# Kernel optimization log

Hardware: AMD Instinct MI355X
Metric: run time of the kernel (lower is better)

The kernel has to match this reference:

```python
import jax, jax.numpy as jnp
import numpy as np


def setup_inputs() -> dict:
    key = jax.random.key(0)
    k1, k2 = jax.random.split(key)
    B, C, H, W = 4, 128, 192, 192
    x = jax.random.normal(k1, (B, C, H, W), dtype=jnp.float32)
    y = jax.random.normal(k2, (B, C, H, W), dtype=jnp.float32)
    return {"x": x, "y": y, "kernel_size": 9, "stride": 1}


def reference(x, y, kernel_size, stride):
    # FlowNet-style correlation volume: for each displacement offset in a
    # kernel_size x kernel_size window (spacing = stride), compute the
    # channel-mean dot product between x and the shifted y.
    # Output: [B, kernel_size**2, H, W]
    B, C, H, W = x.shape
    d = kernel_size // 2          # displacement radius in offset units
    pad = d * stride              # spatial padding so all shifts are valid
    y_pad = jnp.pad(y, ((0, 0), (0, 0), (pad, pad), (pad, pad)))
    inv_c = jnp.float32(1.0 / C)
    outs = []
    # small fixed loop over kernel_size**2 offsets (81 for k=9); each
    # iteration is a fused elementwise-multiply + channel reduction.
    for i in range(kernel_size):
        for j in range(kernel_size):
            ys = jax.lax.dynamic_slice(
                y_pad, (0, 0, i * stride, j * stride), (B, C, H, W))
            outs.append(jnp.sum(x * ys, axis=1) * inv_c)  # [B, H, W]
    return jnp.stack(outs, axis=1)  # [B, k*k, H, W]
```

## Files before the change

kernel.cpp:

```cpp
#include <hip/hip_runtime.h>
#include <hip/hip_bf16.h>

typedef short bf16x8 __attribute__((ext_vector_type(8)));
typedef float f32x4  __attribute__((ext_vector_type(4)));
typedef unsigned short us8 __attribute__((ext_vector_type(8)));

#define NT 1024

__device__ __forceinline__ unsigned short f2bf(float f) {
    __hip_bfloat16 h = __float2bfloat16(f);
    return reinterpret_cast<const unsigned short&>(h);
}

__global__ __launch_bounds__(NT, 4)
void corr_k(const float* __restrict__ x, const float* __restrict__ y,
            float* __restrict__ out)
{
    constexpr int H = 192, W = 192;
    constexpr int plane = H * W;
    constexpr int pl4   = plane * 4;
    constexpr int CHB   = 64 * pl4;

    __shared__ __align__(16) char smem[143360];

    const int bid  = blockIdx.x;
    const int task = (bid & 7) * 144 + (bid >> 3);
    const int ht   = task % 24;
    const int r1   = task / 24;
    const int wt   = r1 % 12;
    const int b    = r1 / 12;
    const int h0 = ht * 8, w0 = wt * 16;

    const int tid  = threadIdx.x;
    const int wid  = tid >> 6;
    const int lane = tid & 63;
    const int lm = lane & 15, lg = lane >> 4;
    const int r = wid >> 1, half = wid & 1, dy0 = half ? 4 : 0;

    const unsigned boff = (unsigned)b * 128u * (unsigned)pl4;

    const char* gptr; char* lptr; int dstride; float okf;
    int lwo[4];
    if (tid < 768) {
        const int cg = tid & 7, w4 = (tid >> 3) % 6, row = tid / 48;
        const int hg = h0 - 4 + row, wg = w0 - 4 + w4 * 4;
        okf = ((hg >= 0) & (hg < H) & (wg >= 0) & (wg <= W - 4)) ? 1.f : 0.f;
        const int hc = min(max(hg, 0), H - 1);
        const int wc = min(max(wg, 0), W - 4);
        gptr = (const char*)y + (boff + (unsigned)(cg * 8) * pl4
                                 + (unsigned)(hc * W + wc) * 4u);
        lptr = smem + row * 3072 + w4 * 512;
        dstride = 49152;
#pragma unroll
        for (int w = 0; w < 4; ++w)
            lwo[w] = w * 128 + ((cg ^ ((w4 * 4 + w) & 7)) << 4);
    } else {
        const int t = tid - 768;
        const int cg = t & 7, w4 = (t >> 3) & 3, row = t >> 5;
        okf = 1.f;
        gptr = (const char*)x + (boff + (unsigned)(cg * 8) * pl4
                                 + (unsigned)((h0 + row) * W + w0 + w4 * 4) * 4u);
        lptr = smem + 98304 + row * 2048 + w4 * 512;
        dstride = 16384;
#pragma unroll
        for (int w = 0; w < 4; ++w)
            lwo[w] = w * 128 + ((cg ^ ((w4 * 4 + w) & 7)) << 4);
    }

    f32x4 pf[8];
    f32x4 acc[5][2];
#pragma unroll
    for (int i = 0; i < 5; ++i) {
        acc[i][0] = (f32x4){0.f, 0.f, 0.f, 0.f};
        acc[i][1] = (f32x4){0.f, 0.f, 0.f, 0.f};
    }

    const int so0 = ((lg ^ (lm & 7)) << 4);
    const int so1 = so0 ^ 64;

    auto STAGE = [&](int ck) {
#pragma unroll
        for (int j = 0; j < 8; ++j)
            pf[j] = *reinterpret_cast<const f32x4*>(gptr + ck * CHB + j * pl4);
    };
    auto CVTW = [&](int ck) {
        char* d = lptr + (ck & 1) * dstride;
#pragma unroll
        for (int w = 0; w < 4; ++w) {
            us8 v = { f2bf(pf[0][w] * okf), f2bf(pf[1][w] * okf),
                      f2bf(pf[2][w] * okf), f2bf(pf[3][w] * okf),
                      f2bf(pf[4][w] * okf), f2bf(pf[5][w] * okf),
                      f2bf(pf[6][w] * okf), f2bf(pf[7][w] * okf) };
            *reinterpret_cast<us8*>(d + lwo[w]) = v;
        }
    };
    auto COMPUTE = [&](int buf) {
        const char* xb = smem + 98304 + buf * 16384 + r * 2048 + lm * 128;
        const bf16x8 a0 = *reinterpret_cast<const bf16x8*>(xb + so0);
        const bf16x8 a1 = *reinterpret_cast<const bf16x8*>(xb + so1);
        const char* yb0 = smem + buf * 49152 + (r + dy0) * 3072 + lm * 128;
#pragma unroll
        for (int i = 0; i < 5; ++i) {
            if (i < 4 || half) {
                const char* yb = yb0 + i * 3072;
                const bf16x8 b00 = *reinterpret_cast<const bf16x8*>(yb + so0);
                const bf16x8 b01 = *reinterpret_cast<const bf16x8*>(yb + 2048 + so0);
                const bf16x8 b10 = *reinterpret_cast<const bf16x8*>(yb + so1);
                const bf16x8 b11 = *reinterpret_cast<const bf16x8*>(yb + 2048 + so1);
                acc[i][0] = __builtin_amdgcn_mfma_f32_16x16x32_bf16(a0, b00, acc[i][0], 0, 0, 0);
                acc[i][1] = __builtin_amdgcn_mfma_f32_16x16x32_bf16(a0, b01, acc[i][1], 0, 0, 0);
                acc[i][0] = __builtin_amdgcn_mfma_f32_16x16x32_bf16(a1, b10, acc[i][0], 0, 0, 0);
                acc[i][1] = __builtin_amdgcn_mfma_f32_16x16x32_bf16(a1, b11, acc[i][1], 0, 0, 0);
            }
        }
    };

    STAGE(0);
    CVTW(0);
    STAGE(1);
    __syncthreads();
    COMPUTE(0);
    CVTW(1);
    __syncthreads();
    COMPUTE(1);

    const float invc = 1.0f / 128.0f;
    float* my = (float*)(smem + 131072) + wid * 192;
    int woff[8];
#pragma unroll
    for (int q = 0; q < 8; ++q) {
        const int nt = q >> 2, j = q & 3;
        const int m = lg * 4 + j;
        const int dxx = lm + nt * 16 - m;
        woff[q] = (dxx >= 0 && dxx <= 8) ? dxx * 17 + m : 160 + (lane & 31);
    }
    int ridx[3], soff[3];
#pragma unroll
    for (int p = 0; p < 3; ++p) {
        const int idx = p * 64 + lane;
        const int dxr = idx >> 4, mr = idx & 15;
        ridx[p] = dxr * 17 + mr;
        soff[p] = dxr * plane + mr;
    }
    float* ob = out + (size_t)b * 81 * plane + (size_t)(h0 + r) * W + w0;
#pragma unroll
    for (int i = 0; i < 5; ++i) {
        if (i < 4 || half) {
            const int dy = dy0 + i;
#pragma unroll
            for (int q = 0; q < 8; ++q)
                my[woff[q]] = acc[i][q >> 2][q & 3] * invc;
            const int dyoff = dy * 9 * plane;
#pragma unroll
            for (int p = 0; p < 3; ++p)
                if (p < 2 || lane < 16)
                    ob[dyoff + soff[p]] = my[ridx[p]];
        }
    }
}

extern "C" void kernel_launch(void* const* d_in, const int* in_sizes, int n_in,
                              void* d_out, int out_size, void* d_ws, size_t ws_size,
                              hipStream_t stream)
{
    const float* x = (const float*)d_in[0];
    const float* y = (const float*)d_in[1];
    float* out = (float*)d_out;
    corr_k<<<1152, NT, 0, stream>>>(x, y, out);
}
```

Before: 232.2 us.

## Halve block size, process two rows per wave, loop channels in 32-chunks

```diff
diff --git a/kernel.cpp b/kernel.cpp
--- a/kernel.cpp
+++ b/kernel.cpp
@@ -3,9 +3,15 @@
 
 typedef short bf16x8 __attribute__((ext_vector_type(8)));
 typedef float f32x4  __attribute__((ext_vector_type(4)));
+typedef float f32x2  __attribute__((ext_vector_type(2)));
 typedef unsigned short us8 __attribute__((ext_vector_type(8)));
 
-#define NT 1024
+#define NT 512
+#define YROW 1936
+#define XBASE 30976
+#define XROW 1296
+#define EPBASE 41344
+#define SMEM_SZ 47488
 
 __device__ __forceinline__ unsigned short f2bf(float f) {
     __hip_bfloat16 h = __float2bfloat16(f);
@@ -18,10 +24,9 @@
 {
     constexpr int H = 192, W = 192;
     constexpr int plane = H * W;
-    constexpr int pl4   = plane * 4;
-    constexpr int CHB   = 64 * pl4;
+    constexpr unsigned PL4 = plane * 4u;
 
-    __shared__ __align__(16) char smem[143360];
+    __shared__ __align__(16) char smem[SMEM_SZ];
 
     const int bid  = blockIdx.x;
     const int task = (bid & 7) * 144 + (bid >> 3);
@@ -32,100 +37,105 @@
     const int h0 = ht * 8, w0 = wt * 16;
 
     const int tid  = threadIdx.x;
-    const int wid  = tid >> 6;
-    const int lane = tid & 63;
+    const int wid  = tid >> 6, lane = tid & 63;
     const int lm = lane & 15, lg = lane >> 4;
-    const int r = wid >> 1, half = wid & 1, dy0 = half ? 4 : 0;
+    const int rp = wid >> 1;
+    const int half = wid & 1;
+    const int dy0  = half ? 4 : 0;
 
-    const unsigned boff = (unsigned)b * 128u * (unsigned)pl4;
+    const unsigned boff = (unsigned)b * 128u * PL4;
 
-    const char* gptr; char* lptr; int dstride; float okf;
-    int lwo[4];
-    if (tid < 768) {
-        const int cg = tid & 7, w4 = (tid >> 3) % 6, row = tid / 48;
-        const int hg = h0 - 4 + row, wg = w0 - 4 + w4 * 4;
-        okf = ((hg >= 0) & (hg < H) & (wg >= 0) & (wg <= W - 4)) ? 1.f : 0.f;
+    const char* gbase; unsigned goff0, goff1; float ok0, ok1; int lbase;
+    if (tid < 384) {
+        const int cg = tid & 3, pq = tid >> 2;
+        const int row = pq / 6, pqi = pq % 6;
+        const int hg = h0 - 4 + row;
         const int hc = min(max(hg, 0), H - 1);
-        const int wc = min(max(wg, 0), W - 4);
-        gptr = (const char*)y + (boff + (unsigned)(cg * 8) * pl4
-                                 + (unsigned)(hc * W + wc) * 4u);
-        lptr = smem + row * 3072 + w4 * 512;
-        dstride = 49152;
-#pragma unroll
-        for (int w = 0; w < 4; ++w)
-            lwo[w] = w * 128 + ((cg ^ ((w4 * 4 + w) & 7)) << 4);
+        const int wg0 = w0 - 4 + pqi * 4;
+        const int wg1 = wg0 + 2;
+        const int wc0 = min(max(wg0, 0), W - 2);
+        const int wc1 = min(max(wg1, 0), W - 2);
+        const bool okr = (hg >= 0) & (hg < H);
+        ok0 = (okr & (wg0 >= 0) & (wg0 < W - 1)) ? 1.f : 0.f;
+        ok1 = (okr & (wg1 >= 0) & (wg1 < W - 1)) ? 1.f : 0.f;
+        gbase = (const char*)y;
+        goff0 = boff + (unsigned)(cg * 8) * PL4 + (unsigned)(hc * W + wc0) * 4u;
+        goff1 = boff + (unsigned)(cg * 8) * PL4 + (unsigned)(hc * W + wc1) * 4u;
+        lbase = row * YROW + pqi * 4 * 80 + cg * 16;
     } else {
-        const int t = tid - 768;
-        const int cg = t & 7, w4 = (t >> 3) & 3, row = t >> 5;
-        okf = 1.f;
-        gptr = (const char*)x + (boff + (unsigned)(cg * 8) * pl4
-                                 + (unsigned)((h0 + row) * W + w0 + w4 * 4) * 4u);
-        lptr = smem + 98304 + row * 2048 + w4 * 512;
-        dstride = 16384;
-#pragma unroll
-        for (int w = 0; w < 4; ++w)
-            lwo[w] = w * 128 + ((cg ^ ((w4 * 4 + w) & 7)) << 4);
+        const int t = tid - 384;
+        const int cg = t & 3, pq = t >> 2;
+        const int row = pq >> 2, pqi = pq & 3;
+        ok0 = ok1 = 1.f;
+        gbase = (const char*)x;
+        const unsigned base = boff + (unsigned)(cg * 8) * PL4
+                            + (unsigned)((h0 + row) * W + w0 + pqi * 4) * 4u;
+        goff0 = base; goff1 = base + 8u;
+        lbase = XBASE + row * XROW + pqi * 4 * 80 + cg * 16;
     }
 
-    f32x4 pf[8];
-    f32x4 acc[5][2];
+    f32x2 pf[8];
+    f32x4 acc[2][5][2];
 #pragma unroll
-    for (int i = 0; i < 5; ++i) {
-        acc[i][0] = (f32x4){0.f, 0.f, 0.f, 0.f};
-        acc[i][1] = (f32x4){0.f, 0.f, 0.f, 0.f};
-    }
+    for (int r = 0; r < 2; ++r)
+#pragma unroll
+        for (int i = 0; i < 5; ++i) {
+            acc[r][i][0] = (f32x4){0.f, 0.f, 0.f, 0.f};
+            acc[r][i][1] = (f32x4){0.f, 0.f, 0.f, 0.f};
+        }
 
-    const int so0 = ((lg ^ (lm & 7)) << 4);
-    const int so1 = so0 ^ 64;
-
-    auto STAGE = [&](int ck) {
+    auto ISSUE = [&](unsigned off) {
 #pragma unroll
         for (int j = 0; j < 8; ++j)
-            pf[j] = *reinterpret_cast<const f32x4*>(gptr + ck * CHB + j * pl4);
+            pf[j] = *reinterpret_cast<const f32x2*>(gbase + off + (unsigned)j * PL4);
     };
-    auto CVTW = [&](int ck) {
-        char* d = lptr + (ck & 1) * dstride;
+    auto CVTW = [&](int bb, float ok) {
 #pragma unroll
-        for (int w = 0; w < 4; ++w) {
-            us8 v = { f2bf(pf[0][w] * okf), f2bf(pf[1][w] * okf),
-                      f2bf(pf[2][w] * okf), f2bf(pf[3][w] * okf),
-                      f2bf(pf[4][w] * okf), f2bf(pf[5][w] * okf),
-                      f2bf(pf[6][w] * okf), f2bf(pf[7][w] * okf) };
-            *reinterpret_cast<us8*>(d + lwo[w]) = v;
+        for (int p = 0; p < 2; ++p) {
+            us8 v = { f2bf(pf[0][p] * ok), f2bf(pf[1][p] * ok),
+                      f2bf(pf[2][p] * ok), f2bf(pf[3][p] * ok),
+                      f2bf(pf[4][p] * ok), f2bf(pf[5][p] * ok),
+                      f2bf(pf[6][p] * ok), f2bf(pf[7][p] * ok) };
+            *reinterpret_cast<us8*>(smem + lbase + (2 * bb + p) * 80) = v;
         }
     };
-    auto COMPUTE = [&](int buf) {
-        const char* xb = smem + 98304 + buf * 16384 + r * 2048 + lm * 128;
-        const bf16x8 a0 = *reinterpret_cast<const bf16x8*>(xb + so0);
-        const bf16x8 a1 = *reinterpret_cast<const bf16x8*>(xb + so1);
-        const char* yb0 = smem + buf * 49152 + (r + dy0) * 3072 + lm * 128;
+    auto COMPUTE = [&]() {
+        const int rb = lm * 80 + lg * 16;
+        const bf16x8 A0 = *reinterpret_cast<const bf16x8*>(
+            smem + XBASE + (2 * rp) * XROW + rb);
+        const bf16x8 A1 = *reinterpret_cast<const bf16x8*>(
+            smem + XBASE + (2 * rp + 1) * XROW + rb);
 #pragma unroll
         for (int i = 0; i < 5; ++i) {
             if (i < 4 || half) {
-                const char* yb = yb0 + i * 3072;
-                const bf16x8 b00 = *reinterpret_cast<const bf16x8*>(yb + so0);
-                const bf16x8 b01 = *reinterpret_cast<const bf16x8*>(yb + 2048 + so0);
-                const bf16x8 b10 = *reinterpret_cast<const bf16x8*>(yb + so1);
-                const bf16x8 b11 = *reinterpret_cast<const bf16x8*>(yb + 2048 + so1);
-                acc[i][0] = __builtin_amdgcn_mfma_f32_16x16x32_bf16(a0, b00, acc[i][0], 0, 0, 0);
-                acc[i][1] = __builtin_amdgcn_mfma_f32_16x16x32_bf16(a0, b01, acc[i][1], 0, 0, 0);
-                acc[i][0] = __builtin_amdgcn_mfma_f32_16x16x32_bf16(a1, b10, acc[i][0], 0, 0, 0);
-                acc[i][1] = __builtin_amdgcn_mfma_f32_16x16x32_bf16(a1, b11, acc[i][1], 0, 0, 0);
+                const char* y0 = smem + (2 * rp + dy0 + i) * YROW + rb;
+                const bf16x8 b00 = *reinterpret_cast<const bf16x8*>(y0);
+                const bf16x8 b01 = *reinterpret_cast<const bf16x8*>(y0 + 16 * 80);
+                const bf16x8 b10 = *reinterpret_cast<const bf16x8*>(y0 + YROW);
+                const bf16x8 b11 = *reinterpret_cast<const bf16x8*>(y0 + YROW + 16 * 80);
+                acc[0][i][0] = __builtin_amdgcn_mfma_f32_16x16x32_bf16(A0, b00, acc[0][i][0], 0, 0, 0);
+                acc[0][i][1] = __builtin_amdgcn_mfma_f32_16x16x32_bf16(A0, b01, acc[0][i][1], 0, 0, 0);
+                acc[1][i][0] = __builtin_amdgcn_mfma_f32_16x16x32_bf16(A1, b10, acc[1][i][0], 0, 0, 0);
+                acc[1][i][1] = __builtin_amdgcn_mfma_f32_16x16x32_bf16(A1, b11, acc[1][i][1], 0, 0, 0);
             }
         }
     };
 
-    STAGE(0);
-    CVTW(0);
-    STAGE(1);
-    __syncthreads();
-    COMPUTE(0);
-    CVTW(1);
-    __syncthreads();
-    COMPUTE(1);
+    ISSUE(goff0);
+#pragma unroll
+    for (int c = 0; c < 4; ++c) {
+        const unsigned co = (unsigned)c * 32u * PL4;
+        CVTW(0, ok0);
+        ISSUE(goff1 + co);
+        CVTW(1, ok1);
+        if (c < 3) ISSUE(goff0 + co + 32u * PL4);
+        __syncthreads();
+        COMPUTE();
+        __syncthreads();
+    }
 
     const float invc = 1.0f / 128.0f;
-    float* my = (float*)(smem + 131072) + wid * 192;
+    float* my = (float*)(smem + EPBASE) + wid * 192;
     int woff[8];
 #pragma unroll
     for (int q = 0; q < 8; ++q) {
@@ -142,19 +152,22 @@
         ridx[p] = dxr * 17 + mr;
         soff[p] = dxr * plane + mr;
     }
-    float* ob = out + (size_t)b * 81 * plane + (size_t)(h0 + r) * W + w0;
 #pragma unroll
-    for (int i = 0; i < 5; ++i) {
-        if (i < 4 || half) {
-            const int dy = dy0 + i;
+    for (int rr = 0; rr < 2; ++rr) {
+        float* ob = out + (size_t)b * 81 * plane + (size_t)(h0 + 2 * rp + rr) * W + w0;
 #pragma unroll
-            for (int q = 0; q < 8; ++q)
-                my[woff[q]] = acc[i][q >> 2][q & 3] * invc;
-            const int dyoff = dy * 9 * plane;
+        for (int i = 0; i < 5; ++i) {
+            if (i < 4 || half) {
+                const int dy = dy0 + i;
 #pragma unroll
-            for (int p = 0; p < 3; ++p)
-                if (p < 2 || lane < 16)
-                    ob[dyoff + soff[p]] = my[ridx[p]];
+                for (int q = 0; q < 8; ++q)
+                    my[woff[q]] = acc[rr][i][q >> 2][q & 3] * invc;
+                const int dyo = dy * 9 * plane;
+#pragma unroll
+                for (int p = 0; p < 3; ++p)
+                    if (p < 2 || lane < 16)
+                        __builtin_nontemporal_store(my[ridx[p]], &ob[dyo + soff[p]]);
+            }
         }
     }
 }
```

Result: slower. 293.2 us (+26.3%).

## Halve block size and stream channels in four 32-wide chunks with one warp per row

Applied to the files above, without the earlier changes.

```diff
diff --git a/kernel.cpp b/kernel.cpp
--- a/kernel.cpp
+++ b/kernel.cpp
@@ -5,7 +5,14 @@
 typedef float f32x4  __attribute__((ext_vector_type(4)));
 typedef unsigned short us8 __attribute__((ext_vector_type(8)));
 
-#define NT 1024
+#define NT 512
+#define YROW 1600
+#define YBUF 25600
+#define XROW 1088
+#define XBASE 51200
+#define XBUF 8704
+#define EPB  68608
+#define SMEM_SZ 74752
 
 __device__ __forceinline__ unsigned short f2bf(float f) {
     __hip_bfloat16 h = __float2bfloat16(f);
@@ -18,114 +25,109 @@
 {
     constexpr int H = 192, W = 192;
     constexpr int plane = H * W;
-    constexpr int pl4   = plane * 4;
-    constexpr int CHB   = 64 * pl4;
+    constexpr unsigned PL4 = plane * 4u;
+    constexpr unsigned CHB = 32u * PL4;
 
-    __shared__ __align__(16) char smem[143360];
+    __shared__ __align__(16) char smem[SMEM_SZ];
 
     const int bid  = blockIdx.x;
     const int task = (bid & 7) * 144 + (bid >> 3);
-    const int ht   = task % 24;
-    const int r1   = task / 24;
-    const int wt   = r1 % 12;
-    const int b    = r1 / 12;
+    const int wt   = task % 12;
+    const int r1   = task / 12;
+    const int ht   = r1 % 24;
+    const int b    = r1 / 24;
     const int h0 = ht * 8, w0 = wt * 16;
 
     const int tid  = threadIdx.x;
-    const int wid  = tid >> 6;
-    const int lane = tid & 63;
+    const int wid  = tid >> 6, lane = tid & 63;
     const int lm = lane & 15, lg = lane >> 4;
-    const int r = wid >> 1, half = wid & 1, dy0 = half ? 4 : 0;
 
-    const unsigned boff = (unsigned)b * 128u * (unsigned)pl4;
+    const unsigned boff = (unsigned)b * 128u * PL4;
 
-    const char* gptr; char* lptr; int dstride; float okf;
-    int lwo[4];
-    if (tid < 768) {
-        const int cg = tid & 7, w4 = (tid >> 3) % 6, row = tid / 48;
+    const char* gb; unsigned goff; float okf; int lbase, bstride, cg;
+    if (tid < 384) {
+        cg = tid & 3;
+        const int w4 = (tid >> 2) % 6, row = tid / 24;
         const int hg = h0 - 4 + row, wg = w0 - 4 + w4 * 4;
         okf = ((hg >= 0) & (hg < H) & (wg >= 0) & (wg <= W - 4)) ? 1.f : 0.f;
         const int hc = min(max(hg, 0), H - 1);
         const int wc = min(max(wg, 0), W - 4);
-        gptr = (const char*)y + (boff + (unsigned)(cg * 8) * pl4
-                                 + (unsigned)(hc * W + wc) * 4u);
-        lptr = smem + row * 3072 + w4 * 512;
-        dstride = 49152;
-#pragma unroll
-        for (int w = 0; w < 4; ++w)
-            lwo[w] = w * 128 + ((cg ^ ((w4 * 4 + w) & 7)) << 4);
+        gb   = (const char*)y;
+        goff = boff + (unsigned)(cg * 8) * PL4 + (unsigned)(hc * W + wc) * 4u;
+        lbase = row * YROW + w4 * 256;
+        bstride = YBUF;
     } else {
-        const int t = tid - 768;
-        const int cg = t & 7, w4 = (t >> 3) & 3, row = t >> 5;
+        const int t = tid - 384;
+        cg = t & 3;
+        const int w4 = (t >> 2) & 3, row = t >> 4;
         okf = 1.f;
-        gptr = (const char*)x + (boff + (unsigned)(cg * 8) * pl4
-                                 + (unsigned)((h0 + row) * W + w0 + w4 * 4) * 4u);
-        lptr = smem + 98304 + row * 2048 + w4 * 512;
-        dstride = 16384;
-#pragma unroll
-        for (int w = 0; w < 4; ++w)
-            lwo[w] = w * 128 + ((cg ^ ((w4 * 4 + w) & 7)) << 4);
+        gb   = (const char*)x;
+        goff = boff + (unsigned)(cg * 8) * PL4
+             + (unsigned)((h0 + row) * W + w0 + w4 * 4) * 4u;
+        lbase = XBASE + row * XROW + w4 * 256;
+        bstride = XBUF;
     }
 
     f32x4 pf[8];
-    f32x4 acc[5][2];
+    f32x4 acc[9][2];
 #pragma unroll
-    for (int i = 0; i < 5; ++i) {
+    for (int i = 0; i < 9; ++i) {
         acc[i][0] = (f32x4){0.f, 0.f, 0.f, 0.f};
         acc[i][1] = (f32x4){0.f, 0.f, 0.f, 0.f};
     }
 
-    const int so0 = ((lg ^ (lm & 7)) << 4);
-    const int so1 = so0 ^ 64;
-
-    auto STAGE = [&](int ck) {
+    auto ISSUE = [&](int c) {
+        const char* p = gb + goff + (unsigned)c * CHB;
 #pragma unroll
         for (int j = 0; j < 8; ++j)
-            pf[j] = *reinterpret_cast<const f32x4*>(gptr + ck * CHB + j * pl4);
+            pf[j] = *reinterpret_cast<const f32x4*>(p + (unsigned)j * PL4);
     };
-    auto CVTW = [&](int ck) {
-        char* d = lptr + (ck & 1) * dstride;
+    auto CVTW = [&](int c) {
+        char* d = smem + lbase + (c & 1) * bstride;
 #pragma unroll
         for (int w = 0; w < 4; ++w) {
             us8 v = { f2bf(pf[0][w] * okf), f2bf(pf[1][w] * okf),
                       f2bf(pf[2][w] * okf), f2bf(pf[3][w] * okf),
                       f2bf(pf[4][w] * okf), f2bf(pf[5][w] * okf),
                       f2bf(pf[6][w] * okf), f2bf(pf[7][w] * okf) };
-            *reinterpret_cast<us8*>(d + lwo[w]) = v;
+            *reinterpret_cast<us8*>(d + w * 64 + ((cg ^ w) << 4)) = v;
         }
     };
-    auto COMPUTE = [&](int buf) {
-        const char* xb = smem + 98304 + buf * 16384 + r * 2048 + lm * 128;
-        const bf16x8 a0 = *reinterpret_cast<const bf16x8*>(xb + so0);
-        const bf16x8 a1 = *reinterpret_cast<const bf16x8*>(xb + so1);
-        const char* yb0 = smem + buf * 49152 + (r + dy0) * 3072 + lm * 128;
+    auto COMPUTE = [&](int c) {
+        const int bs = c & 1;
+        const int ro  = lm * 64 + ((lg ^ (lm & 3)) << 4);
+        const int ro1 = ro + 1024;
+        const bf16x8 A = *reinterpret_cast<const bf16x8*>(
+            smem + XBASE + bs * XBUF + wid * XROW + ro);
+        const char* yb = smem + bs * YBUF + wid * YROW;
 #pragma unroll
-        for (int i = 0; i < 5; ++i) {
-            if (i < 4 || half) {
-                const char* yb = yb0 + i * 3072;
-                const bf16x8 b00 = *reinterpret_cast<const bf16x8*>(yb + so0);
-                const bf16x8 b01 = *reinterpret_cast<const bf16x8*>(yb + 2048 + so0);
-                const bf16x8 b10 = *reinterpret_cast<const bf16x8*>(yb + so1);
-                const bf16x8 b11 = *reinterpret_cast<const bf16x8*>(yb + 2048 + so1);
-                acc[i][0] = __builtin_amdgcn_mfma_f32_16x16x32_bf16(a0, b00, acc[i][0], 0, 0, 0);
-                acc[i][1] = __builtin_amdgcn_mfma_f32_16x16x32_bf16(a0, b01, acc[i][1], 0, 0, 0);
-                acc[i][0] = __builtin_amdgcn_mfma_f32_16x16x32_bf16(a1, b10, acc[i][0], 0, 0, 0);
-                acc[i][1] = __builtin_amdgcn_mfma_f32_16x16x32_bf16(a1, b11, acc[i][1], 0, 0, 0);
-            }
+        for (int i = 0; i < 9; ++i) {
+            const bf16x8 b0 = *reinterpret_cast<const bf16x8*>(yb + i * YROW + ro);
+            const bf16x8 b1 = *reinterpret_cast<const bf16x8*>(yb + i * YROW + ro1);
+            acc[i][0] = __builtin_amdgcn_mfma_f32_16x16x32_bf16(A, b0, acc[i][0], 0, 0, 0);
+            acc[i][1] = __builtin_amdgcn_mfma_f32_16x16x32_bf16(A, b1, acc[i][1], 0, 0, 0);
         }
     };
 
-    STAGE(0);
+    ISSUE(0);
     CVTW(0);
-    STAGE(1);
+    ISSUE(1);
     __syncthreads();
     COMPUTE(0);
     CVTW(1);
+    ISSUE(2);
     __syncthreads();
     COMPUTE(1);
+    CVTW(2);
+    ISSUE(3);
+    __syncthreads();
+    COMPUTE(2);
+    CVTW(3);
+    __syncthreads();
+    COMPUTE(3);
 
     const float invc = 1.0f / 128.0f;
-    float* my = (float*)(smem + 131072) + wid * 192;
+    float* my = (float*)(smem + EPB) + wid * 192;
     int woff[8];
 #pragma unroll
     for (int q = 0; q < 8; ++q) {
@@ -142,20 +144,17 @@
         ridx[p] = dxr * 17 + mr;
         soff[p] = dxr * plane + mr;
     }
-    float* ob = out + (size_t)b * 81 * plane + (size_t)(h0 + r) * W + w0;
+    float* ob = out + (size_t)b * 81 * plane + (size_t)(h0 + wid) * W + w0;
 #pragma unroll
-    for (int i = 0; i < 5; ++i) {
-        if (i < 4 || half) {
-            const int dy = dy0 + i;
+    for (int dy = 0; dy < 9; ++dy) {
 #pragma unroll
-            for (int q = 0; q < 8; ++q)
-                my[woff[q]] = acc[i][q >> 2][q & 3] * invc;
-            const int dyoff = dy * 9 * plane;
+        for (int q = 0; q < 8; ++q)
+            my[woff[q]] = acc[dy][q >> 2][q & 3] * invc;
+        const int dyo = dy * 9 * plane;
 #pragma unroll
-            for (int p = 0; p < 3; ++p)
-                if (p < 2 || lane < 16)
-                    ob[dyoff + soff[p]] = my[ridx[p]];
-        }
+        for (int p = 0; p < 3; ++p)
+            if (p < 2 || lane < 16)
+                ob[dyo + soff[p]] = my[ridx[p]];
     }
 }
 
```

Result: slower. 246.5 us (+6.2%).
